# Performance work log

Hardware: AMD Instinct MI355X
Metric: run time of the kernel (lower is better)

Reference implementation:

```python
import jax, jax.numpy as jnp
import numpy as np

RC = 5.0          # radial cutoff
NB = 8            # number of Gaussian radial basis functions
NPATH = 11        # graph-conv tensor-product paths (in_way, r_way, n_contract)->out_way
NORM_FACTOR = 10.0


def setup_inputs() -> dict:
    key = jax.random.key(0)
    ks = jax.random.split(key, 24)
    N, E, C = 20000, 200000, 32
    s = 1.0 / np.sqrt(C)
    inp = {
        "rij": jax.random.normal(ks[0], (E, 3), jnp.float32) * 1.5,
        "node_x0": jax.random.normal(ks[1], (N, C), jnp.float32),
        "node_x1": jax.random.normal(ks[2], (N, C, 3), jnp.float32),
        "node_x2": jax.random.normal(ks[3], (N, C, 3, 3), jnp.float32),
        "idx_i": jax.random.randint(ks[4], (E,), 0, N, jnp.int32),
        "idx_j": jax.random.randint(ks[5], (E,), 0, N, jnp.int32),
        # radial filter MLP (rbf -> per-path per-channel filters)
        "W_rbf": jax.random.normal(ks[6], (NB, NPATH * C), jnp.float32) / np.sqrt(NB),
        "b_rbf": jax.random.normal(ks[7], (NPATH * C,), jnp.float32) * 0.1,
        # multi-body self-interaction: channel mixing per way + pair-path couplings
        "Wmix0": jax.random.normal(ks[8], (C, C), jnp.float32) * s,
        "Wmix1": jax.random.normal(ks[9], (C, C), jnp.float32) * s,
        "Wmix2": jax.random.normal(ks[10], (C, C), jnp.float32) * s,
        "coupling": jax.random.normal(ks[11], (8, C), jnp.float32) * 0.1,
        # gated nonlinearity params (gates computed from way-0 features)
        "Wg0": jax.random.normal(ks[12], (C, C), jnp.float32) * s,
        "Wg1": jax.random.normal(ks[13], (C, C), jnp.float32) * s,
        "Wg2": jax.random.normal(ks[14], (C, C), jnp.float32) * s,
        "bg0": jnp.zeros((C,), jnp.float32),
        "bg1": jnp.zeros((C,), jnp.float32),
        "bg2": jnp.zeros((C,), jnp.float32),
    }
    return inp


def _forward(rij, node_x0, node_x1, node_x2, idx_i, idx_j,
             W_rbf, b_rbf, Wmix0, Wmix1, Wmix2, coupling,
             Wg0, Wg1, Wg2, bg0, bg1, bg2):
    N, C = node_x0.shape
    # --- radial filters ---
    d = jnp.maximum(jnp.linalg.norm(rij, axis=-1), 1e-6)            # [E]
    rhat = rij / d[:, None]                                         # [E,3]
    centers = jnp.linspace(0.0, RC, NB)
    rbf = jnp.exp(-((d[:, None] - centers) ** 2) / 0.25)            # [E,NB]
    fc = 0.5 * (jnp.cos(jnp.pi * jnp.minimum(d, RC) / RC) + 1.0)    # cosine cutoff
    filt = ((rbf @ W_rbf + b_rbf) * fc[:, None]).reshape(-1, NPATH, C)  # [E,P,C]

    # --- graph conv (conv_mode='node_j'): gather neighbor tensors, tensor-product with rhat ---
    xj0 = node_x0[idx_j]                                            # [E,C]
    xj1 = node_x1[idx_j]                                            # [E,C,3]
    xj2 = node_x2[idx_j]                                            # [E,C,3,3]
    x1r = jnp.einsum('eca,ea->ec', xj1, rhat)                       # v.rhat

    m0 = filt[:, 0] * xj0
    m0 += filt[:, 5] * x1r
    m0 += filt[:, 10] * jnp.einsum('ecab,ea,eb->ec', xj2, rhat, rhat)

    m1 = jnp.einsum('ec,ea->eca', filt[:, 1] * xj0, rhat)
    m1 += filt[:, 3][:, :, None] * xj1
    m1 += jnp.einsum('ec,ea->eca', filt[:, 6] * x1r, rhat)
    m1 += filt[:, 8][:, :, None] * jnp.einsum('ecab,eb->eca', xj2, rhat)

    m2 = jnp.einsum('ec,ea,eb->ecab', filt[:, 2] * xj0, rhat, rhat)
    m2 += jnp.einsum('eca,eb->ecab', filt[:, 4][:, :, None] * xj1, rhat)
    m2 += filt[:, 7][:, :, None, None] * xj2
    m2 += filt[:, 9][:, :, None, None] * jnp.einsum('ecab,eb,ed->ecad', xj2, rhat, rhat)

    # --- scatter-add aggregation per way + normalization ---
    a0 = jax.ops.segment_sum(m0, idx_i, num_segments=N) / NORM_FACTOR
    a1 = jax.ops.segment_sum(m1, idx_i, num_segments=N) / NORM_FACTOR
    a2 = jax.ops.segment_sum(m2, idx_i, num_segments=N) / NORM_FACTOR

    # --- multi-body self-interaction (channel mix + pairwise tensor contractions) ---
    cp = coupling
    y0 = a0 @ Wmix0 \
        + cp[0] * (a0 * a0) \
        + cp[3] * jnp.einsum('nca,nca->nc', a1, a1) \
        + cp[6] * jnp.einsum('ncab,ncab->nc', a2, a2)
    y1 = jnp.einsum('nca,cd->nda', a1, Wmix1) \
        + cp[1][None, :, None] * a0[:, :, None] * a1 \
        + cp[5][None, :, None] * jnp.einsum('ncab,ncb->nca', a2, a1)
    y2 = jnp.einsum('ncab,cd->ndab', a2, Wmix2) \
        + cp[2][None, :, None, None] * a0[:, :, None, None] * a2 \
        + cp[4][None, :, None, None] * jnp.einsum('nca,ncb->ncab', a1, a1) \
        + cp[7][None, :, None, None] * jnp.einsum('ncab,ncbd->ncad', a2, a2)

    # --- gated nonlinearity (scalar channel drives gates for higher ways) ---
    z0 = jax.nn.silu(y0 @ Wg0 + bg0)
    z1 = y1 * jax.nn.silu(y0 @ Wg1 + bg1)[:, :, None]
    z2 = y2 * jax.nn.silu(y0 @ Wg2 + bg2)[:, :, None, None]

    # --- residual add (res_add) ---
    o0 = node_x0 + z0
    o1 = node_x1 + z1
    o2 = node_x2 + z2
    # pack dict {0,1,2} outputs into one array [N,C,1+3+9]
    return jnp.concatenate([o0[:, :, None], o1, o2.reshape(N, C, 9)], axis=-1)


def reference(rij, node_x0, node_x1, node_x2, idx_i, idx_j,
              W_rbf, b_rbf, Wmix0, Wmix1, Wmix2, coupling,
              Wg0, Wg1, Wg2, bg0, bg1, bg2):
    return _forward(rij, node_x0, node_x1, node_x2, idx_i, idx_j,
                    W_rbf, b_rbf, Wmix0, Wmix1, Wmix2, coupling,
                    Wg0, Wg1, Wg2, bg0, bg1, bg2)
```

## Files before the change

kernel.cpp:

```cpp
#include <hip/hip_runtime.h>
#include <cmath>

#define CH 32
#define NBASIS 8
#define NPATH 11
#define NF 13
#define NPF (NF * CH)
#define MAXDEG 40
#define NW 4
#define NWPAIR (NPATH * 4)

typedef unsigned int u32;

__device__ __forceinline__ float silu_f(float x) {
    return x / (1.0f + __expf(-x));
}

__device__ __forceinline__ u32 bf16r(float x) {
    return (__float_as_uint(x) + 0x8000u) >> 16;
}
__device__ __forceinline__ float bf16lo(u32 w) {
    return __uint_as_float(w << 16);
}
__device__ __forceinline__ float bf16hi(u32 w) {
    return __uint_as_float(w & 0xffff0000u);
}

__device__ __forceinline__ void gload_lds16(const void* g, void* l) {
    __builtin_amdgcn_global_load_lds(
        (const __attribute__((address_space(1))) void*)g,
        (__attribute__((address_space(3))) void*)l, 16, 0, 0);
}

__global__ __launch_bounds__(256) void repack_kernel(
    const float* __restrict__ x0,
    const float* __restrict__ x1,
    const float* __restrict__ x2,
    float* __restrict__ xp,
    uint4* __restrict__ xph4,
    int*   __restrict__ cnt,
    int N)
{
    int t = blockIdx.x * 256 + threadIdx.x;
    if (t < N) cnt[t] = 0;
    if (t >= N * CH) return;
    int n = t >> 5, c = t & 31;

    float f[13];
    f[0] = x0[t];
    const float* p1 = x1 + (size_t)t * 3;
#pragma unroll
    for (int a = 0; a < 3; a++) f[1 + a] = p1[a];
    const float* p2 = x2 + (size_t)t * 9;
#pragma unroll
    for (int q = 0; q < 9; q++) f[4 + q] = p2[q];

    float* xpn = xp + (size_t)n * NPF + c;
#pragma unroll
    for (int q = 0; q < 13; q++) xpn[q * CH] = f[q];

    u32 d[8];
#pragma unroll
    for (int qp = 0; qp < 6; qp++)
        d[qp] = bf16r(f[2 * qp]) | (bf16r(f[2 * qp + 1]) << 16);
    d[6] = bf16r(f[12]);
    d[7] = 0u;
    uint4* xo = xph4 + (size_t)t * 2;
    xo[0] = make_uint4(d[0], d[1], d[2], d[3]);
    xo[1] = make_uint4(d[4], d[5], d[6], d[7]);
}

__global__ __launch_bounds__(256) void fill_slots(
    const float* __restrict__ rij,
    const int*   __restrict__ idx_i,
    const int*   __restrict__ idx_j,
    int*    __restrict__ cnt,
    float4* __restrict__ recs,
    int E)
{
    int e = blockIdx.x * 256 + threadIdx.x;
    if (e >= E) return;

    float rx = rij[e * 3 + 0], ry = rij[e * 3 + 1], rz = rij[e * 3 + 2];
    float dn = sqrtf(rx * rx + ry * ry + rz * rz);
    float d = fmaxf(dn, 1e-6f);
    float inv = 1.0f / d;

    float rbf[NBASIS];
#pragma unroll
    for (int k = 0; k < NBASIS; k++) {
        float ck = 5.0f * (float)k / (float)(NBASIS - 1);
        float del = d - ck;
        rbf[k] = __expf(-4.0f * del * del);
    }
    float dc = fminf(d, 5.0f);
    float fc = 0.5f * (__cosf((float)M_PI * dc * 0.2f) + 1.0f);
    float scale = fc * 0.1f;

    int i = idx_i[e];
    int pos = atomicAdd(&cnt[i], 1);
    if (pos >= MAXDEG) return;

    u32 w3  = ((u32)idx_j[e] << 16) | bf16r(scale);
    u32 p01 = bf16r(rbf[0] * scale) | (bf16r(rbf[1] * scale) << 16);
    u32 p23 = bf16r(rbf[2] * scale) | (bf16r(rbf[3] * scale) << 16);
    u32 p45 = bf16r(rbf[4] * scale) | (bf16r(rbf[5] * scale) << 16);
    u32 p67 = bf16r(rbf[6] * scale) | (bf16r(rbf[7] * scale) << 16);

    float4* r = recs + 2 * (size_t)(i * MAXDEG + pos);
    r[0] = make_float4(rx * inv, ry * inv, rz * inv, __uint_as_float(w3));
    r[1] = make_float4(__uint_as_float(p01), __uint_as_float(p23),
                       __uint_as_float(p45), __uint_as_float(p67));
}

__global__ __launch_bounds__(256, 1) void edge_kernel(
    const float4*   __restrict__ recs,
    const uint4*    __restrict__ xph4,
    const int*      __restrict__ cnt,
    const float*    __restrict__ W_rbf,
    const float*    __restrict__ b_rbf,
    float* __restrict__ anode,
    int N)
{
    __shared__ float2 sWP[NWPAIR * CH];
    __shared__ float4 srec[NW][MAXDEG * 2];

    int tid  = threadIdx.x;
    int wid  = tid >> 6;
    int lane = tid & 63;
    int half = lane >> 5;
    int c    = lane & 31;
    int n    = blockIdx.x * NW + wid;
    bool valid = (n < N);
    int nn = valid ? n : (N - 1);

    const char* gbase = (const char*)(recs + 2 * (size_t)nn * MAXDEG);
    {
        char* lbase = (char*)&srec[wid][0];
        gload_lds16(gbase + lane * 16, lbase);
        if (lane < 16)
            gload_lds16(gbase + 1024 + lane * 16, lbase + 1024);
    }

    const u32* recw = (const u32*)gbase;
    u32 w30 = recw[half * 8 + 3];
    u32 w31 = recw[(half + 2) * 8 + 3];
    u32 w32 = recw[(half + 4) * 8 + 3];
    int deg_g = cnt[nn];

#pragma unroll
    for (int i = 0; i < 6; i++) {
        int idx = tid + i * 256;
        if (idx < NWPAIR * CH) {
            int cc = idx & 31, q = idx >> 5, p = q >> 2, t = q & 3;
            sWP[idx] = make_float2(W_rbf[(2 * t) * (NPATH * CH) + p * CH + cc],
                                   W_rbf[(2 * t + 1) * (NPATH * CH) + p * CH + cc]);
        }
    }

    float breg[NPATH];
#pragma unroll
    for (int p = 0; p < NPATH; p++) breg[p] = b_rbf[p * CH + c];

    auto gath = [&](uint4& ga, uint4& gb, u32 w3) {
        int j = (int)(w3 >> 16);
        j = j < N ? j : N - 1;
        const uint4* g = xph4 + (((size_t)j * CH + c) << 1);
        ga = g[0];
        gb = g[1];
    };

    uint4 G0a, G0b, G1a, G1b, G2a, G2b;
    gath(G0a, G0b, w30);
    gath(G1a, G1b, w31);
    gath(G2a, G2b, w32);

    __syncthreads();
    if (!valid) return;

    int deg = deg_g < MAXDEG ? deg_g : MAXDEG;

    int s0 = half, s1 = half + 2, s2 = half + 4;
    bool v0 = s0 < deg, v1 = s1 < deg, v2 = s2 < deg;

    float A0 = 0.0f, A1[3] = {0, 0, 0}, A2[9] = {0, 0, 0, 0, 0, 0, 0, 0, 0};

    const float2* sWPc = sWP + c;

    auto compute = [&](float4 ra, float4 rb4, uint4 ga, uint4 gb) {
        float G[13];
        G[0]  = bf16lo(ga.x); G[1]  = bf16hi(ga.x);
        G[2]  = bf16lo(ga.y); G[3]  = bf16hi(ga.y);
        G[4]  = bf16lo(ga.z); G[5]  = bf16hi(ga.z);
        G[6]  = bf16lo(ga.w); G[7]  = bf16hi(ga.w);
        G[8]  = bf16lo(gb.x); G[9]  = bf16hi(gb.x);
        G[10] = bf16lo(gb.y); G[11] = bf16hi(gb.y);
        G[12] = bf16lo(gb.z);

        float scale = bf16lo(__float_as_uint(ra.w));
        u32 pb[4] = { __float_as_uint(rb4.x), __float_as_uint(rb4.y),
                      __float_as_uint(rb4.z), __float_as_uint(rb4.w) };

        float fv[NPATH];
#pragma unroll
        for (int p = 0; p < NPATH; p++) {
            float acc = scale * breg[p];
#pragma unroll
            for (int t = 0; t < 4; t++) {
                float2 w = sWPc[(p * 4 + t) * CH];
                acc = fmaf(bf16lo(pb[t]), w.x, acc);
                acc = fmaf(bf16hi(pb[t]), w.y, acc);
            }
            fv[p] = acc;
        }

        float hv[3] = {ra.x, ra.y, ra.z};
        float xj0 = G[0];
        float xv[3] = {G[1], G[2], G[3]};
        float x1r = xv[0] * hv[0] + xv[1] * hv[1] + xv[2] * hv[2];
        float x2r[3];
#pragma unroll
        for (int a = 0; a < 3; a++)
            x2r[a] = G[4 + a * 3 + 0] * hv[0] + G[4 + a * 3 + 1] * hv[1]
                   + G[4 + a * 3 + 2] * hv[2];
        float x2rr = x2r[0] * hv[0] + x2r[1] * hv[1] + x2r[2] * hv[2];

        A0 += fv[0] * xj0 + fv[5] * x1r + fv[10] * x2rr;

        float s01 = fv[1] * xj0 + fv[6] * x1r;
#pragma unroll
        for (int a = 0; a < 3; a++)
            A1[a] += s01 * hv[a] + fv[3] * xv[a] + fv[8] * x2r[a];

        float f2x = fv[2] * xj0;
#pragma unroll
        for (int a = 0; a < 3; a++) {
            float w = f2x * hv[a] + fv[4] * xv[a] + fv[9] * x2r[a];
#pragma unroll
            for (int b = 0; b < 3; b++)
                A2[a * 3 + b] += w * hv[b] + fv[7] * G[4 + a * 3 + b];
        }
    };

    const float4* sr = srec[wid];

    while (v0) {
        bool n0 = (s0 + 6 < deg);
        bool n1 = v1 && (s1 + 6 < deg);
        bool n2 = v2 && (s2 + 6 < deg);

        float4 ra0 = sr[2 * s0], rb0 = sr[2 * s0 + 1];
        int t0 = s0 + 6 < MAXDEG ? s0 + 6 : MAXDEG - 1;
        u32 w0n = __float_as_uint(sr[2 * t0].w);
        float4 ra1, rb1, ra2, rb2;
        u32 w1n = 0, w2n = 0;
        if (v1) {
            ra1 = sr[2 * s1]; rb1 = sr[2 * s1 + 1];
            int t1 = s1 + 6 < MAXDEG ? s1 + 6 : MAXDEG - 1;
            w1n = __float_as_uint(sr[2 * t1].w);
        }
        if (v2) {
            ra2 = sr[2 * s2]; rb2 = sr[2 * s2 + 1];
            int t2 = s2 + 6 < MAXDEG ? s2 + 6 : MAXDEG - 1;
            w2n = __float_as_uint(sr[2 * t2].w);
        }

        compute(ra0, rb0, G0a, G0b);
        if (n0) gath(G0a, G0b, w0n);
        s0 += 6; v0 = n0;

        if (v1) {
            compute(ra1, rb1, G1a, G1b);
            if (n1) gath(G1a, G1b, w1n);
            s1 += 6; v1 = n1;
        }
        if (v2) {
            compute(ra2, rb2, G2a, G2b);
            if (n2) gath(G2a, G2b, w2n);
            s2 += 6; v2 = n2;
        }
    }

    A0 += __shfl_xor(A0, 32);
#pragma unroll
    for (int a = 0; a < 3; a++) A1[a] += __shfl_xor(A1[a], 32);
#pragma unroll
    for (int q = 0; q < 9; q++) A2[q] += __shfl_xor(A2[q], 32);

    float* an = anode + (size_t)n * NPF;
    if (half == 0) {
        an[c] = A0;
#pragma unroll
        for (int a = 0; a < 3; a++) an[(1 + a) * CH + c] = A1[a];
    } else {
#pragma unroll
        for (int q = 0; q < 9; q++) an[(4 + q) * CH + c] = A2[q];
    }
}

__global__ __launch_bounds__(256) void node_update(
    const float* __restrict__ anode,
    const float* __restrict__ xp,
    const float* __restrict__ Wmix0, const float* __restrict__ Wmix1, const float* __restrict__ Wmix2,
    const float* __restrict__ coupling,
    const float* __restrict__ Wg0, const float* __restrict__ Wg1, const float* __restrict__ Wg2,
    const float* __restrict__ bg0, const float* __restrict__ bg1, const float* __restrict__ bg2,
    float* __restrict__ out, int N)
{
    __shared__ float sW[6][CH * CH];
    __shared__ float sA[8 * NPF];
    __shared__ float sy0[8][CH];
    __shared__ float ob[8 * NPF];

    int tid  = threadIdx.x;
    int nl   = tid >> 5;
    int d    = tid & 31;
    int nbase = blockIdx.x * 8;
    int n    = nbase + nl;

#pragma unroll
    for (int r = 0; r < 4; r++) {
        int idx = r * 256 + tid;
        sW[0][idx] = Wmix0[idx];
        sW[1][idx] = Wmix1[idx];
        sW[2][idx] = Wmix2[idx];
        sW[3][idx] = Wg0[idx];
        sW[4][idx] = Wg1[idx];
        sW[5][idx] = Wg2[idx];
    }
    int limit = (N - nbase) * NPF;
    if (limit > 8 * NPF) limit = 8 * NPF;
    {
        const float* ab = anode + (size_t)nbase * NPF;
#pragma unroll
        for (int r = 0; r < 13; r++) {
            int idx = r * 256 + tid;
            sA[idx] = (idx < limit) ? ab[idx] : 0.0f;
        }
    }
    __syncthreads();

    const float* An = sA + nl * NPF;

    float a0d = An[0 * CH + d];
    float a1d[3], a2d[9];
#pragma unroll
    for (int a = 0; a < 3; a++) a1d[a] = An[(1 + a) * CH + d];
#pragma unroll
    for (int q = 0; q < 9; q++) a2d[q] = An[(4 + q) * CH + d];

    float y0 = 0.0f;
#pragma unroll 8
    for (int cc = 0; cc < CH; cc++)
        y0 = fmaf(An[cc], sW[0][cc * CH + d], y0);
    {
        float cp0 = coupling[0 * CH + d], cp3 = coupling[3 * CH + d], cp6 = coupling[6 * CH + d];
        float n1v = a1d[0] * a1d[0] + a1d[1] * a1d[1] + a1d[2] * a1d[2];
        float n2v = 0.0f;
#pragma unroll
        for (int q = 0; q < 9; q++) n2v = fmaf(a2d[q], a2d[q], n2v);
        y0 += cp0 * a0d * a0d + cp3 * n1v + cp6 * n2v;
    }
    sy0[nl][d] = y0;
    __syncthreads();

    float y1[3] = {0, 0, 0};
    float y2[9] = {0, 0, 0, 0, 0, 0, 0, 0, 0};
    float g0 = bg0[d], g1 = bg1[d], g2 = bg2[d];
#pragma unroll 4
    for (int cc = 0; cc < CH; cc++) {
        float w1 = sW[1][cc * CH + d];
        float w2 = sW[2][cc * CH + d];
#pragma unroll
        for (int a = 0; a < 3; a++) y1[a] = fmaf(An[(1 + a) * CH + cc], w1, y1[a]);
#pragma unroll
        for (int q = 0; q < 9; q++) y2[q] = fmaf(An[(4 + q) * CH + cc], w2, y2[q]);
        float yv = sy0[nl][cc];
        g0 = fmaf(yv, sW[3][cc * CH + d], g0);
        g1 = fmaf(yv, sW[4][cc * CH + d], g1);
        g2 = fmaf(yv, sW[5][cc * CH + d], g2);
    }

    {
        float cp1 = coupling[1 * CH + d], cp5 = coupling[5 * CH + d];
#pragma unroll
        for (int a = 0; a < 3; a++) {
            float a2a1 = a2d[a * 3 + 0] * a1d[0] + a2d[a * 3 + 1] * a1d[1] + a2d[a * 3 + 2] * a1d[2];
            y1[a] += cp1 * a0d * a1d[a] + cp5 * a2a1;
        }
        float cp2 = coupling[2 * CH + d], cp4 = coupling[4 * CH + d], cp7 = coupling[7 * CH + d];
#pragma unroll
        for (int a = 0; a < 3; a++) {
#pragma unroll
            for (int b = 0; b < 3; b++) {
                float a2a2 = a2d[a * 3 + 0] * a2d[0 * 3 + b] + a2d[a * 3 + 1] * a2d[1 * 3 + b]
                           + a2d[a * 3 + 2] * a2d[2 * 3 + b];
                y2[a * 3 + b] += cp2 * a0d * a2d[a * 3 + b] + cp4 * a1d[a] * a1d[b] + cp7 * a2a2;
            }
        }
    }

    g0 = silu_f(g0);
    g1 = silu_f(g1);
    g2 = silu_f(g2);

    {
        const float* xn = xp + (size_t)n * NPF;
        float* o = ob + nl * NPF + d * NF;
        const float* xs = xp + (size_t)(n < N ? n : N - 1) * NPF;
        o[0] = xs[0 * CH + d] + g0;
#pragma unroll
        for (int a = 0; a < 3; a++)
            o[1 + a] = xs[(1 + a) * CH + d] + y1[a] * g1;
#pragma unroll
        for (int q = 0; q < 9; q++)
            o[4 + q] = xs[(4 + q) * CH + d] + y2[q] * g2;
        (void)xn;
    }
    __syncthreads();

    float* op = out + (size_t)nbase * NPF;
#pragma unroll
    for (int r = 0; r < 13; r++) {
        int idx = r * 256 + tid;
        if (idx < limit) op[idx] = ob[idx];
    }
}

extern "C" void kernel_launch(void* const* d_in, const int* in_sizes, int n_in,
                              void* d_out, int out_size, void* d_ws, size_t ws_size,
                              hipStream_t stream) {
    const float* rij      = (const float*)d_in[0];
    const float* x0       = (const float*)d_in[1];
    const float* x1       = (const float*)d_in[2];
    const float* x2       = (const float*)d_in[3];
    const int*   idx_i    = (const int*)d_in[4];
    const int*   idx_j    = (const int*)d_in[5];
    const float* W_rbf    = (const float*)d_in[6];
    const float* b_rbf    = (const float*)d_in[7];
    const float* Wmix0    = (const float*)d_in[8];
    const float* Wmix1    = (const float*)d_in[9];
    const float* Wmix2    = (const float*)d_in[10];
    const float* coupling = (const float*)d_in[11];
    const float* Wg0      = (const float*)d_in[12];
    const float* Wg1      = (const float*)d_in[13];
    const float* Wg2      = (const float*)d_in[14];
    const float* bg0      = (const float*)d_in[15];
    const float* bg1      = (const float*)d_in[16];
    const float* bg2      = (const float*)d_in[17];

    int E = in_sizes[4];
    int N = in_sizes[1] / CH;

    float4* recs  = (float4*)d_ws;
    float*  xp    = (float*)(recs + 2 * (size_t)N * MAXDEG);
    uint4*  xph4  = (uint4*)(xp + (size_t)N * NPF);
    int*    cnt   = (int*)(xph4 + (size_t)N * CH * 2);
    float*  anode = (float*)d_out;

    int ablocks = (N * CH + 255) / 256;
    repack_kernel<<<ablocks, 256, 0, stream>>>(x0, x1, x2, xp, xph4, cnt, N);

    int eblocks = (E + 255) / 256;
    fill_slots<<<eblocks, 256, 0, stream>>>(rij, idx_i, idx_j, cnt, recs, E);

    edge_kernel<<<(N + NW - 1) / NW, 256, 0, stream>>>(recs, xph4, cnt,
                                                       W_rbf, b_rbf, anode, N);

    node_update<<<(N + 7) / 8, 256, 0, stream>>>(anode, xp,
                                                 Wmix0, Wmix1, Wmix2, coupling,
                                                 Wg0, Wg1, Wg2, bg0, bg1, bg2,
                                                 (float*)d_out, N);
}
```

Before: 252.0 us.

## Drop fp32 planar node copy and batch three edge slots' filter computation

The repack kernel no longer writes a planar fp32 copy of the node features. node_update now reads the residual inputs straight from the original x0/x1/x2 arrays, which removes a full write and later read of N*C*13 floats. The edge loop also now computes the radial filters for all three in-flight slots together with shared LDS weight loads. Invalid slots are masked by zeroing their inputs instead of taking branches. The cost is extra register pressure and wasted arithmetic on masked slots, and the residual reads in node_update are now strided.

```diff
diff --git a/kernel.cpp b/kernel.cpp
--- a/kernel.cpp
+++ b/kernel.cpp
@@ -36,7 +36,6 @@
     const float* __restrict__ x0,
     const float* __restrict__ x1,
     const float* __restrict__ x2,
-    float* __restrict__ xp,
     uint4* __restrict__ xph4,
     int*   __restrict__ cnt,
     int N)
@@ -44,7 +43,6 @@
     int t = blockIdx.x * 256 + threadIdx.x;
     if (t < N) cnt[t] = 0;
     if (t >= N * CH) return;
-    int n = t >> 5, c = t & 31;
 
     float f[13];
     f[0] = x0[t];
@@ -54,10 +52,6 @@
     const float* p2 = x2 + (size_t)t * 9;
 #pragma unroll
     for (int q = 0; q < 9; q++) f[4 + q] = p2[q];
-
-    float* xpn = xp + (size_t)n * NPF + c;
-#pragma unroll
-    for (int q = 0; q < 13; q++) xpn[q * CH] = f[q];
 
     u32 d[8];
 #pragma unroll
@@ -180,14 +174,16 @@
 
     int deg = deg_g < MAXDEG ? deg_g : MAXDEG;
 
-    int s0 = half, s1 = half + 2, s2 = half + 4;
-    bool v0 = s0 < deg, v1 = s1 < deg, v2 = s2 < deg;
+    int s0 = half;
+    bool v0 = s0 < deg, v1 = s0 + 2 < deg, v2 = s0 + 4 < deg;
 
     float A0 = 0.0f, A1[3] = {0, 0, 0}, A2[9] = {0, 0, 0, 0, 0, 0, 0, 0, 0};
 
     const float2* sWPc = sWP + c;
-
-    auto compute = [&](float4 ra, float4 rb4, uint4 ga, uint4 gb) {
+    const float4* sr = srec[wid];
+
+    auto tp = [&](const float* hv, const uint4& ga, const uint4& gb,
+                  const float* fv) {
         float G[13];
         G[0]  = bf16lo(ga.x); G[1]  = bf16hi(ga.x);
         G[2]  = bf16lo(ga.y); G[3]  = bf16hi(ga.y);
@@ -197,24 +193,6 @@
         G[10] = bf16lo(gb.y); G[11] = bf16hi(gb.y);
         G[12] = bf16lo(gb.z);
 
-        float scale = bf16lo(__float_as_uint(ra.w));
-        u32 pb[4] = { __float_as_uint(rb4.x), __float_as_uint(rb4.y),
-                      __float_as_uint(rb4.z), __float_as_uint(rb4.w) };
-
-        float fv[NPATH];
-#pragma unroll
-        for (int p = 0; p < NPATH; p++) {
-            float acc = scale * breg[p];
-#pragma unroll
-            for (int t = 0; t < 4; t++) {
-                float2 w = sWPc[(p * 4 + t) * CH];
-                acc = fmaf(bf16lo(pb[t]), w.x, acc);
-                acc = fmaf(bf16hi(pb[t]), w.y, acc);
-            }
-            fv[p] = acc;
-        }
-
-        float hv[3] = {ra.x, ra.y, ra.z};
         float xj0 = G[0];
         float xv[3] = {G[1], G[2], G[3]};
         float x1r = xv[0] * hv[0] + xv[1] * hv[1] + xv[2] * hv[2];
@@ -242,43 +220,66 @@
         }
     };
 
-    const float4* sr = srec[wid];
-
     while (v0) {
-        bool n0 = (s0 + 6 < deg);
-        bool n1 = v1 && (s1 + 6 < deg);
-        bool n2 = v2 && (s2 + 6 < deg);
-
-        float4 ra0 = sr[2 * s0], rb0 = sr[2 * s0 + 1];
-        int t0 = s0 + 6 < MAXDEG ? s0 + 6 : MAXDEG - 1;
-        u32 w0n = __float_as_uint(sr[2 * t0].w);
-        float4 ra1, rb1, ra2, rb2;
-        u32 w1n = 0, w2n = 0;
-        if (v1) {
-            ra1 = sr[2 * s1]; rb1 = sr[2 * s1 + 1];
-            int t1 = s1 + 6 < MAXDEG ? s1 + 6 : MAXDEG - 1;
-            w1n = __float_as_uint(sr[2 * t1].w);
-        }
-        if (v2) {
-            ra2 = sr[2 * s2]; rb2 = sr[2 * s2 + 1];
-            int t2 = s2 + 6 < MAXDEG ? s2 + 6 : MAXDEG - 1;
-            w2n = __float_as_uint(sr[2 * t2].w);
-        }
-
-        compute(ra0, rb0, G0a, G0b);
-        if (n0) gath(G0a, G0b, w0n);
-        s0 += 6; v0 = n0;
-
-        if (v1) {
-            compute(ra1, rb1, G1a, G1b);
-            if (n1) gath(G1a, G1b, w1n);
-            s1 += 6; v1 = n1;
-        }
-        if (v2) {
-            compute(ra2, rb2, G2a, G2b);
-            if (n2) gath(G2a, G2b, w2n);
-            s2 += 6; v2 = n2;
-        }
+        int t1 = s0 + 2;
+        int t2 = s0 + 4 < MAXDEG - 1 ? s0 + 4 : MAXDEG - 1;
+        float4 ra0 = sr[2 * s0], rb40 = sr[2 * s0 + 1];
+        float4 ra1 = sr[2 * t1], rb41 = sr[2 * t1 + 1];
+        float4 ra2 = sr[2 * t2], rb42 = sr[2 * t2 + 1];
+
+        int u0 = s0 + 6  < MAXDEG - 1 ? s0 + 6  : MAXDEG - 1;
+        int u1 = s0 + 8  < MAXDEG - 1 ? s0 + 8  : MAXDEG - 1;
+        int u2 = s0 + 10 < MAXDEG - 1 ? s0 + 10 : MAXDEG - 1;
+        u32 wn0 = __float_as_uint(sr[2 * u0].w);
+        u32 wn1 = __float_as_uint(sr[2 * u1].w);
+        u32 wn2 = __float_as_uint(sr[2 * u2].w);
+
+        float sc0 = v0 ? bf16lo(__float_as_uint(ra0.w)) : 0.0f;
+        float sc1 = v1 ? bf16lo(__float_as_uint(ra1.w)) : 0.0f;
+        float sc2 = v2 ? bf16lo(__float_as_uint(ra2.w)) : 0.0f;
+        float hv0[3] = {v0 ? ra0.x : 0.0f, v0 ? ra0.y : 0.0f, v0 ? ra0.z : 0.0f};
+        float hv1[3] = {v1 ? ra1.x : 0.0f, v1 ? ra1.y : 0.0f, v1 ? ra1.z : 0.0f};
+        float hv2[3] = {v2 ? ra2.x : 0.0f, v2 ? ra2.y : 0.0f, v2 ? ra2.z : 0.0f};
+        u32 pb0[4] = {v0 ? __float_as_uint(rb40.x) : 0u, v0 ? __float_as_uint(rb40.y) : 0u,
+                      v0 ? __float_as_uint(rb40.z) : 0u, v0 ? __float_as_uint(rb40.w) : 0u};
+        u32 pb1[4] = {v1 ? __float_as_uint(rb41.x) : 0u, v1 ? __float_as_uint(rb41.y) : 0u,
+                      v1 ? __float_as_uint(rb41.z) : 0u, v1 ? __float_as_uint(rb41.w) : 0u};
+        u32 pb2[4] = {v2 ? __float_as_uint(rb42.x) : 0u, v2 ? __float_as_uint(rb42.y) : 0u,
+                      v2 ? __float_as_uint(rb42.z) : 0u, v2 ? __float_as_uint(rb42.w) : 0u};
+
+        float rf0[NBASIS], rf1[NBASIS], rf2[NBASIS];
+#pragma unroll
+        for (int t = 0; t < 4; t++) {
+            rf0[2 * t] = bf16lo(pb0[t]); rf0[2 * t + 1] = bf16hi(pb0[t]);
+            rf1[2 * t] = bf16lo(pb1[t]); rf1[2 * t + 1] = bf16hi(pb1[t]);
+            rf2[2 * t] = bf16lo(pb2[t]); rf2[2 * t + 1] = bf16hi(pb2[t]);
+        }
+
+        float fv0[NPATH], fv1[NPATH], fv2[NPATH];
+#pragma unroll
+        for (int p = 0; p < NPATH; p++) {
+            float a0 = sc0 * breg[p], a1 = sc1 * breg[p], a2 = sc2 * breg[p];
+#pragma unroll
+            for (int t = 0; t < 4; t++) {
+                float2 w = sWPc[(p * 4 + t) * CH];
+                a0 = fmaf(rf0[2 * t], w.x, a0); a0 = fmaf(rf0[2 * t + 1], w.y, a0);
+                a1 = fmaf(rf1[2 * t], w.x, a1); a1 = fmaf(rf1[2 * t + 1], w.y, a1);
+                a2 = fmaf(rf2[2 * t], w.x, a2); a2 = fmaf(rf2[2 * t + 1], w.y, a2);
+            }
+            fv0[p] = a0; fv1[p] = a1; fv2[p] = a2;
+        }
+
+        tp(hv0, G0a, G0b, fv0);
+        tp(hv1, G1a, G1b, fv1);
+        tp(hv2, G2a, G2b, fv2);
+
+        bool n0v = s0 + 6 < deg;
+        bool n1v = s0 + 8 < deg;
+        bool n2v = s0 + 10 < deg;
+        if (n0v) gath(G0a, G0b, wn0);
+        if (n1v) gath(G1a, G1b, wn1);
+        if (n2v) gath(G2a, G2b, wn2);
+        s0 += 6; v0 = n0v; v1 = n1v; v2 = n2v;
     }
 
     A0 += __shfl_xor(A0, 32);
@@ -300,7 +301,9 @@
 
 __global__ __launch_bounds__(256) void node_update(
     const float* __restrict__ anode,
-    const float* __restrict__ xp,
+    const float* __restrict__ x0,
+    const float* __restrict__ x1,
+    const float* __restrict__ x2,
     const float* __restrict__ Wmix0, const float* __restrict__ Wmix1, const float* __restrict__ Wmix2,
     const float* __restrict__ coupling,
     const float* __restrict__ Wg0, const float* __restrict__ Wg1, const float* __restrict__ Wg2,
@@ -317,6 +320,7 @@
     int d    = tid & 31;
     int nbase = blockIdx.x * 8;
     int n    = nbase + nl;
+    int nsafe = n < N ? n : N - 1;
 
 #pragma unroll
     for (int r = 0; r < 4; r++) {
@@ -405,17 +409,17 @@
     g2 = silu_f(g2);
 
     {
-        const float* xn = xp + (size_t)n * NPF;
+        const float* xs0 = x0 + (size_t)nsafe * CH;
+        const float* xs1 = x1 + ((size_t)nsafe * CH + d) * 3;
+        const float* xs2 = x2 + ((size_t)nsafe * CH + d) * 9;
         float* o = ob + nl * NPF + d * NF;
-        const float* xs = xp + (size_t)(n < N ? n : N - 1) * NPF;
-        o[0] = xs[0 * CH + d] + g0;
+        o[0] = xs0[d] + g0;
 #pragma unroll
         for (int a = 0; a < 3; a++)
-            o[1 + a] = xs[(1 + a) * CH + d] + y1[a] * g1;
+            o[1 + a] = xs1[a] + y1[a] * g1;
 #pragma unroll
         for (int q = 0; q < 9; q++)
-            o[4 + q] = xs[(4 + q) * CH + d] + y2[q] * g2;
-        (void)xn;
+            o[4 + q] = xs2[q] + y2[q] * g2;
     }
     __syncthreads();
 
@@ -453,13 +457,12 @@
     int N = in_sizes[1] / CH;
 
     float4* recs  = (float4*)d_ws;
-    float*  xp    = (float*)(recs + 2 * (size_t)N * MAXDEG);
-    uint4*  xph4  = (uint4*)(xp + (size_t)N * NPF);
+    uint4*  xph4  = (uint4*)(recs + 2 * (size_t)N * MAXDEG);
     int*    cnt   = (int*)(xph4 + (size_t)N * CH * 2);
     float*  anode = (float*)d_out;
 
     int ablocks = (N * CH + 255) / 256;
-    repack_kernel<<<ablocks, 256, 0, stream>>>(x0, x1, x2, xp, xph4, cnt, N);
+    repack_kernel<<<ablocks, 256, 0, stream>>>(x0, x1, x2, xph4, cnt, N);
 
     int eblocks = (E + 255) / 256;
     fill_slots<<<eblocks, 256, 0, stream>>>(rij, idx_i, idx_j, cnt, recs, E);
@@ -467,7 +470,7 @@
     edge_kernel<<<(N + NW - 1) / NW, 256, 0, stream>>>(recs, xph4, cnt,
                                                        W_rbf, b_rbf, anode, N);
 
-    node_update<<<(N + 7) / 8, 256, 0, stream>>>(anode, xp,
+    node_update<<<(N + 7) / 8, 256, 0, stream>>>(anode, x0, x1, x2,
                                                  Wmix0, Wmix1, Wmix2, coupling,
                                                  Wg0, Wg1, Wg2, bg0, bg1, bg2,
                                                  (float*)d_out, N);
```

New measurement: 299.6 us. 18.9% more time.
